# Performance work log

Measured on AMD Instinct MI355X. Metric: run time of the kernel, lower is better.

Reference implementation:

```python
import jax, jax.numpy as jnp
import numpy as np
from jax import lax


def _depthwise_conv1d(x, w, b):
    # x: [B, L, D]; w: [D, 1, KW]; b: [D]
    # Mirrors torch nn.Conv1d(D, D, kernel_size=4, groups=D, padding=3): output length L + 3.
    D = x.shape[-1]
    xt = jnp.transpose(x, (0, 2, 1))  # [B, D, L]
    out = lax.conv_general_dilated(
        xt, w, window_strides=(1,), padding=[(3, 3)],
        feature_group_count=D, dimension_numbers=('NCH', 'OIH', 'NCH'))
    return jnp.transpose(out + b[None, :, None], (0, 2, 1))  # [B, L+3, D]


def _forward(x, a_hat, W_U, W_B, b_B, W_C, b_C, W_d1, b_d1, W_d2, b_d2, D_skip, conv_w, conv_b):
    xc = _depthwise_conv1d(x, conv_w, conv_b)            # [B, Lc, D], Lc = L + 3
    Bsz, Lc, Dm = xc.shape
    S = a_hat.shape[0]
    # selective parameters (torch Linear: y = x @ W.T + b)
    dt_feat = jax.nn.silu(xc @ W_d1.T + b_d1)            # [B, Lc, R]
    delta = jax.nn.softplus(dt_feat @ W_d2.T + b_d2)     # [B, Lc, 1]
    logA = -jnp.exp(a_hat)                               # [S], log(A) <= 0
    A_t = jnp.exp(delta * logA)                          # [B, Lc, S] discretized transition
    u_t = xc @ W_U.T                                     # [B, Lc, S]
    B_t = (xc @ W_B.T + b_B) * u_t                       # [B, Lc, S]
    C_t = xc @ W_C.T + b_C                               # [B, Lc, S]

    # selective scan: h_t = A_t * h_{t-1} + B_t * u_t ; y_t = <C_t, h_t> + D_skip * u_t
    # state h is per-(batch, channel d): [B, D, S]
    def step(h, inp):
        A_l, B_l, C_l, u_l = inp                         # [B,S],[B,S],[B,S],[B,D]
        h = A_l[:, None, :] * h + B_l[:, None, :] * u_l[:, :, None]  # [B, D, S]
        y = jnp.einsum('bds,bs->bd', h, C_l) + D_skip[None, :] * u_l
        return h, y

    h0 = jnp.zeros((Bsz, Dm, S), dtype=xc.dtype)
    _, ys = lax.scan(step, h0, (jnp.swapaxes(A_t, 0, 1), jnp.swapaxes(B_t, 0, 1),
                                jnp.swapaxes(C_t, 0, 1), jnp.swapaxes(xc, 0, 1)))
    return jnp.swapaxes(ys, 0, 1)                        # [B, Lc, D]


def setup_inputs() -> dict:
    key = jax.random.key(0)
    ks = jax.random.split(key, 10)
    B, L, D, S, R, KW = 4, 2048, 1024, 64, 4, 4
    f = jnp.float32
    sc = 0.02
    return {
        'x': jax.random.normal(ks[0], (B, L, D), f),
        'a_hat': jax.random.normal(ks[1], (S,), f),
        'W_U': jax.random.normal(ks[2], (S, D), f) * sc,
        'W_B': jax.random.normal(ks[3], (S, D), f) * sc,
        'b_B': jnp.zeros((S,), f),
        'W_C': jax.random.normal(ks[4], (S, D), f) * sc,
        'b_C': jnp.zeros((S,), f),
        'W_d1': jax.random.normal(ks[5], (R, D), f) * sc,
        'b_d1': jnp.zeros((R,), f),
        'W_d2': jax.random.normal(ks[6], (1, R), f) * sc,
        'b_d2': jnp.zeros((1,), f),
        'D_skip': jax.random.normal(ks[7], (D,), f),
        'conv_w': jax.random.normal(ks[8], (D, 1, KW), f) * 0.25,
        'conv_b': jnp.zeros((D,), f),
    }


def reference(x, a_hat, W_U, W_B, b_B, W_C, b_C, W_d1, b_d1, W_d2, b_d2, D_skip, conv_w, conv_b):
    return _forward(x, a_hat, W_U, W_B, b_B, W_C, b_C, W_d1, b_d1, W_d2, b_d2, D_skip, conv_w, conv_b)
```

## Files before the change

### kernel.cpp

```cpp
#include <hip/hip_runtime.h>
#include <hip/hip_bf16.h>

namespace {
constexpr int kB   = 4;
constexpr int kL   = 2048;
constexpr int kLc  = 2051;
constexpr int kD   = 1024;
constexpr int kS   = 64;
constexpr int kM   = kB * kLc;
constexpr int kNR  = 256;
constexpr int kQ   = 32;
constexpr int kTC  = (kLc + kQ - 1) / kQ;
constexpr int kGA  = 514;
constexpr int kGT  = 16384;
}

typedef __attribute__((ext_vector_type(8))) short bf16x8;
typedef __attribute__((ext_vector_type(4))) float f32x4;
typedef __attribute__((ext_vector_type(8))) unsigned short u16x8;

__device__ __forceinline__ float siluf_(float v) {
  return v / (1.f + expf(-v));
}
__device__ __forceinline__ float softplusf_(float v) {
  return (v > 20.f) ? v : log1pf(expf(v));
}
__device__ __forceinline__ unsigned short f2bf_(float f) {
  unsigned u = __float_as_uint(f);
  unsigned r = u + 0x7FFF + ((u >> 16) & 1);
  return (unsigned short)(r >> 16);
}
__device__ __forceinline__ float bf2f_(unsigned short u) {
  return __uint_as_float(((unsigned)u) << 16);
}

__global__ __launch_bounds__(256) void wcat_kernel(
    const float* __restrict__ W_U, const float* __restrict__ W_B,
    const float* __restrict__ W_C, const float* __restrict__ W_d1,
    unsigned short* __restrict__ wcp, unsigned short* __restrict__ xcp) {
  int g = blockIdx.x;
  int kq = blockIdx.y;
  int tid = threadIdx.x;
  int c8 = tid & 15, r = tid >> 4;
  int n = g * 16 + r;
  int k = kq * 128 + c8 * 8;
  const float* src = nullptr;
  if (n < 64)        src = W_U + (size_t)n * kD;
  else if (n < 128)  src = W_B + (size_t)(n - 64) * kD;
  else if (n < 192)  src = W_C + (size_t)(n - 128) * kD;
  else if (n < 196)  src = W_d1 + (size_t)(n - 192) * kD;
  u16x8 o;
#pragma unroll
  for (int j = 0; j < 8; ++j) o[j] = src ? f2bf_(src[k + j]) : (unsigned short)0;
  size_t dst = (size_t)g * kGT + (size_t)(k >> 5) * 512 + r * 32 + (k & 31);
  *(u16x8*)(wcp + dst) = o;
  if (kq == 0) {
    u16x8 z = {0, 0, 0, 0, 0, 0, 0, 0};
    size_t off = (size_t)512 * kGT + ((size_t)g * 256 + tid) * 8;
    *(u16x8*)(xcp + off) = z;
  }
}

__global__ __launch_bounds__(256) void conv_kernel(
    const float* __restrict__ x, const float* __restrict__ cw,
    const float* __restrict__ cb, unsigned short* __restrict__ xcp,
    unsigned short* __restrict__ xT) {
  __shared__ unsigned short tileT[kQ][136];

  int tid = threadIdx.x;
  int bc = blockIdx.x;
  int d0 = blockIdx.y * 128;
  int b = bc / kTC, c = bc % kTC;
  int t0 = c * kQ;
  int dl = tid & 127, tg = tid >> 7;
  int d = d0 + dl;

  float4 wv = *(const float4*)(cw + (size_t)d * 4);
  float bias = cb[d];
  int tstart = t0 + tg * 16;

  const float* xb = x + (size_t)b * kL * kD + d;
  auto ldx = [&](int t) -> float {
    return (t >= 0 && t < kL) ? xb[(size_t)t * kD] : 0.f;
  };
  float xm3 = ldx(tstart - 3);
  float xm2 = ldx(tstart - 2);
  float xm1 = ldx(tstart - 1);

  unsigned short vals[16];
#pragma unroll
  for (int j = 0; j < 16; ++j) {
    int t = tstart + j;
    float x0 = ldx(t);
    float o = bias + wv.x * xm3 + wv.y * xm2 + wv.z * xm1 + wv.w * x0;
    vals[j] = (t < kLc) ? f2bf_(o) : (unsigned short)0;
    tileT[tg * 16 + j][dl] = vals[j];
    xm3 = xm2; xm2 = xm1; xm1 = x0;
  }
#pragma unroll
  for (int j = 0; j < 16; ++j) {
    int t = tstart + j;
    if (t < kLc) {
      int bt = b * kLc + t;
      size_t po = (size_t)(bt >> 4) * kGT + (size_t)(d >> 5) * 512 +
                  (size_t)(bt & 15) * 32 + (d & 31);
      xcp[po] = vals[j];
    }
  }
  __syncthreads();
  {
    int d_l = tid >> 1, th = tid & 1;
    u16x8 o0, o1;
#pragma unroll
    for (int j = 0; j < 8; ++j) {
      o0[j] = tileT[th * 16 + j][d_l];
      o1[j] = tileT[th * 16 + 8 + j][d_l];
    }
    unsigned short* dst = xT + ((size_t)bc * kD + d0 + d_l) * kQ + th * 16;
    *(u16x8*)dst = o0;
    *(u16x8*)(dst + 8) = o1;
  }
}

__global__ __launch_bounds__(256) void gemm_mfma_kernel(
    const unsigned short* __restrict__ xcp,
    const unsigned short* __restrict__ wcp, float* __restrict__ raw) {
  int tid = threadIdx.x;
  int w = tid >> 6, lane = tid & 63;
  int m0 = blockIdx.x * 32 + (w >> 1) * 16;
  int n0 = blockIdx.y * 128 + (w & 1) * 64;
  int l15 = lane & 15, lk = lane >> 4;

  const unsigned short* ap =
      xcp + (size_t)(blockIdx.x * 2 + (w >> 1)) * kGT + l15 * 32 + lk * 8;
  const unsigned short* bp =
      wcp + (size_t)(blockIdx.y * 8 + (w & 1) * 4) * kGT + l15 * 32 + lk * 8;

  f32x4 acc0 = {0.f, 0.f, 0.f, 0.f}, acc1 = acc0, acc2 = acc0, acc3 = acc0;

  bf16x8 a  = *(const bf16x8*)(ap);
  bf16x8 b0 = *(const bf16x8*)(bp + (size_t)0 * kGT);
  bf16x8 b1 = *(const bf16x8*)(bp + (size_t)1 * kGT);
  bf16x8 b2 = *(const bf16x8*)(bp + (size_t)2 * kGT);
  bf16x8 b3 = *(const bf16x8*)(bp + (size_t)3 * kGT);

#pragma unroll 4
  for (int kt = 1; kt < 32; ++kt) {
    bf16x8 an  = *(const bf16x8*)(ap + kt * 512);
    bf16x8 b0n = *(const bf16x8*)(bp + (size_t)0 * kGT + kt * 512);
    bf16x8 b1n = *(const bf16x8*)(bp + (size_t)1 * kGT + kt * 512);
    bf16x8 b2n = *(const bf16x8*)(bp + (size_t)2 * kGT + kt * 512);
    bf16x8 b3n = *(const bf16x8*)(bp + (size_t)3 * kGT + kt * 512);
    acc0 = __builtin_amdgcn_mfma_f32_16x16x32_bf16(a, b0, acc0, 0, 0, 0);
    acc1 = __builtin_amdgcn_mfma_f32_16x16x32_bf16(a, b1, acc1, 0, 0, 0);
    acc2 = __builtin_amdgcn_mfma_f32_16x16x32_bf16(a, b2, acc2, 0, 0, 0);
    acc3 = __builtin_amdgcn_mfma_f32_16x16x32_bf16(a, b3, acc3, 0, 0, 0);
    a = an; b0 = b0n; b1 = b1n; b2 = b2n; b3 = b3n;
  }
  acc0 = __builtin_amdgcn_mfma_f32_16x16x32_bf16(a, b0, acc0, 0, 0, 0);
  acc1 = __builtin_amdgcn_mfma_f32_16x16x32_bf16(a, b1, acc1, 0, 0, 0);
  acc2 = __builtin_amdgcn_mfma_f32_16x16x32_bf16(a, b2, acc2, 0, 0, 0);
  acc3 = __builtin_amdgcn_mfma_f32_16x16x32_bf16(a, b3, acc3, 0, 0, 0);

  int crow0 = m0 + lk * 4;
  f32x4 accs[4] = {acc0, acc1, acc2, acc3};
#pragma unroll
  for (int nf = 0; nf < 4; ++nf) {
    int col = n0 + nf * 16 + l15;
#pragma unroll
    for (int r = 0; r < 4; ++r) {
      int row = crow0 + r;
      if (row < kM) raw[(size_t)row * kNR + col] = accs[nf][r];
    }
  }
}

__global__ __launch_bounds__(256) void passA_kernel(
    const float* __restrict__ raw,
    const float* __restrict__ b_B, const float* __restrict__ b_C,
    const float* __restrict__ b_d1, const float* __restrict__ W_d2,
    const float* __restrict__ b_d2, const float* __restrict__ a_hat,
    unsigned short* __restrict__ Gm, unsigned short* __restrict__ Ctb,
    unsigned short* __restrict__ Bpre, float* __restrict__ dec) {
  __shared__ __align__(16) float Cfl[32][68];
  __shared__ __align__(16) float BulT[64][36];
  __shared__ float deltal[32];
  __shared__ float Dloc[32];
  __shared__ float logAl[64];

  int tid = threadIdx.x;
  int bc = blockIdx.x;
  int b = bc / kTC, c = bc % kTC;
  int t0 = c * kQ;
  int clen = min(kQ, kLc - t0);

  if (tid < 64) logAl[tid] = -expf(a_hat[tid]);
  if (tid >= 64 && tid < 96) {
    int t = tid - 64;
    float r0 = 0.f, r1 = 0.f, r2 = 0.f, r3 = 0.f;
    if (t < clen) {
      const float* rp = raw + (size_t)(b * kLc + t0 + t) * kNR + 192;
      r0 = rp[0]; r1 = rp[1]; r2 = rp[2]; r3 = rp[3];
    }
    float f0 = siluf_(r0 + b_d1[0]);
    float f1 = siluf_(r1 + b_d1[1]);
    float f2 = siluf_(r2 + b_d1[2]);
    float f3 = siluf_(r3 + b_d1[3]);
    float z = fmaf(f0, W_d2[0],
              fmaf(f1, W_d2[1], fmaf(f2, W_d2[2], fmaf(f3, W_d2[3], b_d2[0]))));
    deltal[t] = softplusf_(z);
  }
  for (int p = 0; p < 8; ++p) {
    int idx = p * 256 + tid;
    int t = idx >> 6, s = idx & 63;
    float u = 0.f, rb = 0.f, rc = 0.f;
    if (t < clen) {
      const float* rp = raw + (size_t)(b * kLc + t0 + t) * kNR;
      u = rp[s]; rb = rp[64 + s]; rc = rp[128 + s];
    }
    BulT[s][t] = (rb + b_B[s]) * u;
    Cfl[t][s] = rc + b_C[s];
  }
  __syncthreads();
  if (tid < 32) {
    float sum = 0.f;
    for (int j = 0; j <= tid; ++j) sum += deltal[j];
    Dloc[tid] = sum;
  }
  __syncthreads();
  float Dend = Dloc[31];

  for (int p = 0; p < 8; ++p) {
    int idx = p * 256 + tid;
    int t = idx >> 6, s = idx & 63;
    Ctb[(size_t)bc * 2048 + t * kS + s] =
        f2bf_(Cfl[t][s] * __expf(Dloc[t] * logAl[s]));
  }
  for (int p = 0; p < 8; ++p) {
    int idx = p * 256 + tid;
    int s = idx >> 5, tau = idx & 31;
    Bpre[(size_t)bc * 2048 + s * kQ + tau] =
        f2bf_(BulT[s][tau] * __expf((Dend - Dloc[tau]) * logAl[s]));
  }
  if (tid < 64) dec[(size_t)bc * kS + tid] = __expf(Dend * logAl[tid]);
  for (int p = 0; p < 4; ++p) {
    int idx = p * 256 + tid;
    int t = idx >> 5, tau = idx & 31;
    float g = 0.f;
    if (tau <= t) {
      float dd = Dloc[t] - Dloc[tau];
      for (int s = 0; s < 64; ++s)
        g = fmaf(Cfl[t][s] * BulT[s][tau], __expf(dd * logAl[s]), g);
    }
    Gm[((size_t)bc * 32 + t) * kQ + tau] = f2bf_(g);
  }
}

__global__ __launch_bounds__(256) void scT_kernel(
    const unsigned short* __restrict__ Bpre, const unsigned short* __restrict__ xT,
    unsigned short* __restrict__ ScT) {
  __shared__ __align__(16) unsigned short Bprel[64][40];
  int tid = threadIdx.x;
  int bc = blockIdx.x;
  int dq = blockIdx.y;
  {
    int s = tid >> 2, c8 = (tid & 3) * 8;
    *(u16x8*)&Bprel[s][c8] = *(const u16x8*)(Bpre + (size_t)bc * 2048 + s * kQ + c8);
  }
  __syncthreads();
  int w = tid >> 6, lane = tid & 63;
  int l15 = lane & 15, lk = lane >> 4;
  bf16x8 bfr[4];
#pragma unroll
  for (int st = 0; st < 4; ++st)
    bfr[st] = *(const bf16x8*)&Bprel[st * 16 + l15][lk * 8];
  const unsigned short* xTb = xT + (size_t)bc * kD * kQ;
  unsigned short* so = ScT + (size_t)bc * kD * kS;
#pragma unroll
  for (int mt = 0; mt < 4; ++mt) {
    int d0t = dq * 256 + (w * 4 + mt) * 16;
    bf16x8 af = *(const bf16x8*)(xTb + (size_t)(d0t + l15) * kQ + lk * 8);
    f32x4 acc[4];
#pragma unroll
    for (int st = 0; st < 4; ++st) {
      f32x4 z = {0.f, 0.f, 0.f, 0.f};
      acc[st] = __builtin_amdgcn_mfma_f32_16x16x32_bf16(af, bfr[st], z, 0, 0, 0);
    }
#pragma unroll
    for (int st = 0; st < 4; ++st)
#pragma unroll
      for (int r = 0; r < 4; ++r)
        so[(size_t)(d0t + lk * 4 + r) * kS + st * 16 + l15] = f2bf_(acc[st][r]);
  }
}

__global__ __launch_bounds__(256) void chscan_kernel(
    const float* __restrict__ dec, unsigned short* __restrict__ Sc) {
  int bk = blockIdx.x >> 7;
  int part = blockIdx.x & 127;
  int p = part * 256 + threadIdx.x;
  int flat = p * 2;
  int s0 = flat & 63;
  const size_t cstride = (size_t)kS * kD;
  size_t base = (size_t)bk * kTC * cstride + flat;
  const float* decb = dec + (size_t)bk * kTC * kS + s0;
  float r0 = 0.f, r1 = 0.f;
  for (int c0 = 0; c0 < kTC; c0 += 16) {
    int n = kTC - c0;
    if (n > 16) n = 16;
    unsigned v[16];
    float2 dd[16];
#pragma unroll
    for (int j = 0; j < 16; ++j) {
      if (j < n) {
        v[j] = *(const unsigned*)(Sc + base + (size_t)(c0 + j) * cstride);
        dd[j] = *(const float2*)(decb + (size_t)(c0 + j) * kS);
      }
    }
#pragma unroll
    for (int j = 0; j < 16; ++j) {
      if (j < n) {
        unsigned ost = (unsigned)f2bf_(r0) | ((unsigned)f2bf_(r1) << 16);
        *(unsigned*)(Sc + base + (size_t)(c0 + j) * cstride) = ost;
        r0 = fmaf(dd[j].x, r0, bf2f_((unsigned short)(v[j] & 0xFFFF)));
        r1 = fmaf(dd[j].y, r1, bf2f_((unsigned short)(v[j] >> 16)));
      }
    }
  }
}

__global__ __launch_bounds__(256) void passB_kernel(
    const unsigned short* __restrict__ Gm, const unsigned short* __restrict__ Ctb,
    const unsigned short* __restrict__ xT, const unsigned short* __restrict__ hT,
    const float* __restrict__ D_skip, float* __restrict__ out) {
  int tid = threadIdx.x;
  int bc = blockIdx.x;
  int quarter = blockIdx.y;
  int b = bc / kTC, c = bc % kTC;
  int t0c = c * kQ;
  int clen = min(kQ, kLc - t0c);
  int w = tid >> 6, lane = tid & 63;
  int l15 = lane & 15, lk = lane >> 4;

  const unsigned short* Gb = Gm + (size_t)bc * 32 * kQ;
  bf16x8 aG0 = *(const bf16x8*)(Gb + (size_t)l15 * kQ + lk * 8);
  bf16x8 aG1 = *(const bf16x8*)(Gb + (size_t)(16 + l15) * kQ + lk * 8);
  const unsigned short* Cb = Ctb + (size_t)bc * 2048;
  bf16x8 aC0l = *(const bf16x8*)(Cb + (size_t)l15 * kS + lk * 8);
  bf16x8 aC0h = *(const bf16x8*)(Cb + (size_t)l15 * kS + 32 + lk * 8);
  bf16x8 aC1l = *(const bf16x8*)(Cb + (size_t)(16 + l15) * kS + lk * 8);
  bf16x8 aC1h = *(const bf16x8*)(Cb + (size_t)(16 + l15) * kS + 32 + lk * 8);

  const unsigned short* xTb = xT + (size_t)bc * kD * kQ;
  const unsigned short* hTb = hT + (size_t)bc * kD * kS;
  size_t rowbase = (size_t)b * kLc + t0c;
  int dbase = quarter * 256 + w * 64;

#pragma unroll
  for (int nt = 0; nt < 4; ++nt) {
    int d = dbase + nt * 16 + l15;
    bf16x8 bX  = *(const bf16x8*)(xTb + (size_t)d * kQ + lk * 8);
    bf16x8 bHl = *(const bf16x8*)(hTb + (size_t)d * kS + lk * 8);
    bf16x8 bHh = *(const bf16x8*)(hTb + (size_t)d * kS + 32 + lk * 8);
    f32x4 z = {0.f, 0.f, 0.f, 0.f};
    f32x4 accA = __builtin_amdgcn_mfma_f32_16x16x32_bf16(aC0l, bHl, z, 0, 0, 0);
    accA = __builtin_amdgcn_mfma_f32_16x16x32_bf16(aC0h, bHh, accA, 0, 0, 0);
    accA = __builtin_amdgcn_mfma_f32_16x16x32_bf16(aG0, bX, accA, 0, 0, 0);
    f32x4 accB = __builtin_amdgcn_mfma_f32_16x16x32_bf16(aC1l, bHl, z, 0, 0, 0);
    accB = __builtin_amdgcn_mfma_f32_16x16x32_bf16(aC1h, bHh, accB, 0, 0, 0);
    accB = __builtin_amdgcn_mfma_f32_16x16x32_bf16(aG1, bX, accB, 0, 0, 0);

    float ds = D_skip[d];
    ushort4 xa = *(const ushort4*)(xTb + (size_t)d * kQ + lk * 4);
    ushort4 xb = *(const ushort4*)(xTb + (size_t)d * kQ + 16 + lk * 4);
    const unsigned short* xap = (const unsigned short*)&xa;
    const unsigned short* xbp = (const unsigned short*)&xb;
#pragma unroll
    for (int r = 0; r < 4; ++r) {
      int t = lk * 4 + r;
      if (t < clen)
        out[(rowbase + t) * kD + d] = fmaf(ds, bf2f_(xap[r]), accA[r]);
      int t2 = 16 + lk * 4 + r;
      if (t2 < clen)
        out[(rowbase + t2) * kD + d] = fmaf(ds, bf2f_(xbp[r]), accB[r]);
    }
  }
}

extern "C" void kernel_launch(void* const* d_in, const int* in_sizes, int n_in,
                              void* d_out, int out_size, void* d_ws, size_t ws_size,
                              hipStream_t stream) {
  const float* x      = (const float*)d_in[0];
  const float* a_hat  = (const float*)d_in[1];
  const float* W_U    = (const float*)d_in[2];
  const float* W_B    = (const float*)d_in[3];
  const float* b_B    = (const float*)d_in[4];
  const float* W_C    = (const float*)d_in[5];
  const float* b_C    = (const float*)d_in[6];
  const float* W_d1   = (const float*)d_in[7];
  const float* b_d1   = (const float*)d_in[8];
  const float* W_d2   = (const float*)d_in[9];
  const float* b_d2   = (const float*)d_in[10];
  const float* D_skip = (const float*)d_in[11];
  const float* conv_w = (const float*)d_in[12];
  const float* conv_b = (const float*)d_in[13];
  float* out = (float*)d_out;

  char* w = (char*)d_ws;
  auto nextp = [&](size_t bytes) {
    char* p = w;
    w += (bytes + 255) & ~(size_t)255;
    return p;
  };
  unsigned short* xcp  = (unsigned short*)nextp((size_t)kGA * kGT * 2);
  unsigned short* wcp  = (unsigned short*)nextp((size_t)16 * kGT * 2);
  unsigned short* xT   = (unsigned short*)nextp((size_t)kB * kTC * kD * kQ * 2);
  float*          raw  = (float*)nextp((size_t)kM * kNR * 4);
  unsigned short* Gm   = (unsigned short*)nextp((size_t)kB * kTC * 32 * kQ * 2);
  unsigned short* Ctb  = (unsigned short*)nextp((size_t)kB * kTC * 2048 * 2);
  unsigned short* Bpre = (unsigned short*)nextp((size_t)kB * kTC * 2048 * 2);
  float*          dec  = (float*)nextp((size_t)kB * kTC * kS * 4);
  unsigned short* ScT  = (unsigned short*)nextp((size_t)kB * kTC * kD * kS * 2);

  dim3 wgrid(16, 8);
  wcat_kernel<<<wgrid, 256, 0, stream>>>(W_U, W_B, W_C, W_d1, wcp, xcp);

  dim3 cgrid(kB * kTC, kD / 128);
  conv_kernel<<<cgrid, 256, 0, stream>>>(x, conv_w, conv_b, xcp, xT);

  dim3 ggrid((kM + 31) / 32, 2);
  gemm_mfma_kernel<<<ggrid, 256, 0, stream>>>(xcp, wcp, raw);

  passA_kernel<<<kB * kTC, 256, 0, stream>>>(
      raw, b_B, b_C, b_d1, W_d2, b_d2, a_hat, Gm, Ctb, Bpre, dec);

  dim3 sgrid(kB * kTC, 4);
  scT_kernel<<<sgrid, 256, 0, stream>>>(Bpre, xT, ScT);

  chscan_kernel<<<kB * 128, 256, 0, stream>>>(dec, ScT);

  dim3 bgrid(kB * kTC, 4);
  passB_kernel<<<bgrid, 256, 0, stream>>>(Gm, Ctb, xT, ScT, D_skip, out);
}
```

Baseline: 111.1 us.

## Fold weight packing into conv kernel and widen GEMM N-tile to full width

Removes the separate weight-conversion launch by giving the conv kernel an extra grid row that packs the weights to bf16 and zeroes the padding rows of the packed activation buffer. The zeroing is narrowed to only the rows conv does not write. The GEMM now covers all 256 output columns per block: each wave holds 8 accumulators instead of 4, so every A fragment is loaded once instead of twice across blocks. This raises register pressure and halves the GEMM grid, which can lower occupancy.

```diff
diff --git a/kernel.cpp b/kernel.cpp
--- a/kernel.cpp
+++ b/kernel.cpp
@@ -34,40 +34,48 @@
   return __uint_as_float(((unsigned)u) << 16);
 }
 
-__global__ __launch_bounds__(256) void wcat_kernel(
-    const float* __restrict__ W_U, const float* __restrict__ W_B,
-    const float* __restrict__ W_C, const float* __restrict__ W_d1,
-    unsigned short* __restrict__ wcp, unsigned short* __restrict__ xcp) {
-  int g = blockIdx.x;
-  int kq = blockIdx.y;
-  int tid = threadIdx.x;
-  int c8 = tid & 15, r = tid >> 4;
-  int n = g * 16 + r;
-  int k = kq * 128 + c8 * 8;
-  const float* src = nullptr;
-  if (n < 64)        src = W_U + (size_t)n * kD;
-  else if (n < 128)  src = W_B + (size_t)(n - 64) * kD;
-  else if (n < 192)  src = W_C + (size_t)(n - 128) * kD;
-  else if (n < 196)  src = W_d1 + (size_t)(n - 192) * kD;
-  u16x8 o;
-#pragma unroll
-  for (int j = 0; j < 8; ++j) o[j] = src ? f2bf_(src[k + j]) : (unsigned short)0;
-  size_t dst = (size_t)g * kGT + (size_t)(k >> 5) * 512 + r * 32 + (k & 31);
-  *(u16x8*)(wcp + dst) = o;
-  if (kq == 0) {
-    u16x8 z = {0, 0, 0, 0, 0, 0, 0, 0};
-    size_t off = (size_t)512 * kGT + ((size_t)g * 256 + tid) * 8;
-    *(u16x8*)(xcp + off) = z;
-  }
-}
-
 __global__ __launch_bounds__(256) void conv_kernel(
     const float* __restrict__ x, const float* __restrict__ cw,
     const float* __restrict__ cb, unsigned short* __restrict__ xcp,
-    unsigned short* __restrict__ xT) {
+    unsigned short* __restrict__ xT,
+    const float* __restrict__ W_U, const float* __restrict__ W_B,
+    const float* __restrict__ W_C, const float* __restrict__ W_d1,
+    unsigned short* __restrict__ wcp) {
   __shared__ unsigned short tileT[kQ][136];
 
   int tid = threadIdx.x;
+  if (blockIdx.y == 8) {
+    int bx = blockIdx.x;
+    if (bx < 128) {
+      int g = bx >> 3, kq = bx & 7;
+      int c8 = tid & 15, r = tid >> 4;
+      int n = g * 16 + r;
+      int k = kq * 128 + c8 * 8;
+      const float* src = nullptr;
+      if (n < 64)        src = W_U + (size_t)n * kD;
+      else if (n < 128)  src = W_B + (size_t)(n - 64) * kD;
+      else if (n < 192)  src = W_C + (size_t)(n - 128) * kD;
+      else if (n < 196)  src = W_d1 + (size_t)(n - 192) * kD;
+      u16x8 o;
+#pragma unroll
+      for (int j = 0; j < 8; ++j)
+        o[j] = src ? f2bf_(src[k + j]) : (unsigned short)0;
+      size_t dst = (size_t)g * kGT + (size_t)(k >> 5) * 512 + r * 32 + (k & 31);
+      *(u16x8*)(wcp + dst) = o;
+    } else if (bx < 136) {
+      u16x8 z = {0, 0, 0, 0, 0, 0, 0, 0};
+      size_t off = (size_t)513 * kGT + (size_t)(bx - 128) * 2048 + (size_t)tid * 8;
+      *(u16x8*)(xcp + off) = z;
+    } else if (bx < 138) {
+      int i = (bx - 136) * 256 + tid;
+      int kt = i >> 4, rr = (i >> 2) & 3, k8 = i & 3;
+      u16x8 z = {0, 0, 0, 0, 0, 0, 0, 0};
+      size_t off = (size_t)512 * kGT + (size_t)kt * 512 + (12 + rr) * 32 + k8 * 8;
+      *(u16x8*)(xcp + off) = z;
+    }
+    return;
+  }
+
   int bc = blockIdx.x;
   int d0 = blockIdx.y * 128;
   int b = bc / kTC, c = bc % kTC;
@@ -128,49 +136,49 @@
   int tid = threadIdx.x;
   int w = tid >> 6, lane = tid & 63;
   int m0 = blockIdx.x * 32 + (w >> 1) * 16;
-  int n0 = blockIdx.y * 128 + (w & 1) * 64;
+  int n0 = (w & 1) * 128;
   int l15 = lane & 15, lk = lane >> 4;
 
   const unsigned short* ap =
       xcp + (size_t)(blockIdx.x * 2 + (w >> 1)) * kGT + l15 * 32 + lk * 8;
   const unsigned short* bp =
-      wcp + (size_t)(blockIdx.y * 8 + (w & 1) * 4) * kGT + l15 * 32 + lk * 8;
-
-  f32x4 acc0 = {0.f, 0.f, 0.f, 0.f}, acc1 = acc0, acc2 = acc0, acc3 = acc0;
-
-  bf16x8 a  = *(const bf16x8*)(ap);
-  bf16x8 b0 = *(const bf16x8*)(bp + (size_t)0 * kGT);
-  bf16x8 b1 = *(const bf16x8*)(bp + (size_t)1 * kGT);
-  bf16x8 b2 = *(const bf16x8*)(bp + (size_t)2 * kGT);
-  bf16x8 b3 = *(const bf16x8*)(bp + (size_t)3 * kGT);
-
-#pragma unroll 4
+      wcp + (size_t)((w & 1) * 8) * kGT + l15 * 32 + lk * 8;
+
+  f32x4 acc[8];
+#pragma unroll
+  for (int nf = 0; nf < 8; ++nf) acc[nf] = f32x4{0.f, 0.f, 0.f, 0.f};
+
+  bf16x8 a = *(const bf16x8*)(ap);
+  bf16x8 bfr[8];
+#pragma unroll
+  for (int nf = 0; nf < 8; ++nf)
+    bfr[nf] = *(const bf16x8*)(bp + (size_t)nf * kGT);
+
   for (int kt = 1; kt < 32; ++kt) {
-    bf16x8 an  = *(const bf16x8*)(ap + kt * 512);
-    bf16x8 b0n = *(const bf16x8*)(bp + (size_t)0 * kGT + kt * 512);
-    bf16x8 b1n = *(const bf16x8*)(bp + (size_t)1 * kGT + kt * 512);
-    bf16x8 b2n = *(const bf16x8*)(bp + (size_t)2 * kGT + kt * 512);
-    bf16x8 b3n = *(const bf16x8*)(bp + (size_t)3 * kGT + kt * 512);
-    acc0 = __builtin_amdgcn_mfma_f32_16x16x32_bf16(a, b0, acc0, 0, 0, 0);
-    acc1 = __builtin_amdgcn_mfma_f32_16x16x32_bf16(a, b1, acc1, 0, 0, 0);
-    acc2 = __builtin_amdgcn_mfma_f32_16x16x32_bf16(a, b2, acc2, 0, 0, 0);
-    acc3 = __builtin_amdgcn_mfma_f32_16x16x32_bf16(a, b3, acc3, 0, 0, 0);
-    a = an; b0 = b0n; b1 = b1n; b2 = b2n; b3 = b3n;
-  }
-  acc0 = __builtin_amdgcn_mfma_f32_16x16x32_bf16(a, b0, acc0, 0, 0, 0);
-  acc1 = __builtin_amdgcn_mfma_f32_16x16x32_bf16(a, b1, acc1, 0, 0, 0);
-  acc2 = __builtin_amdgcn_mfma_f32_16x16x32_bf16(a, b2, acc2, 0, 0, 0);
-  acc3 = __builtin_amdgcn_mfma_f32_16x16x32_bf16(a, b3, acc3, 0, 0, 0);
+    bf16x8 an = *(const bf16x8*)(ap + kt * 512);
+    bf16x8 bn[8];
+#pragma unroll
+    for (int nf = 0; nf < 8; ++nf)
+      bn[nf] = *(const bf16x8*)(bp + (size_t)nf * kGT + kt * 512);
+#pragma unroll
+    for (int nf = 0; nf < 8; ++nf)
+      acc[nf] = __builtin_amdgcn_mfma_f32_16x16x32_bf16(a, bfr[nf], acc[nf], 0, 0, 0);
+    a = an;
+#pragma unroll
+    for (int nf = 0; nf < 8; ++nf) bfr[nf] = bn[nf];
+  }
+#pragma unroll
+  for (int nf = 0; nf < 8; ++nf)
+    acc[nf] = __builtin_amdgcn_mfma_f32_16x16x32_bf16(a, bfr[nf], acc[nf], 0, 0, 0);
 
   int crow0 = m0 + lk * 4;
-  f32x4 accs[4] = {acc0, acc1, acc2, acc3};
-#pragma unroll
-  for (int nf = 0; nf < 4; ++nf) {
+#pragma unroll
+  for (int nf = 0; nf < 8; ++nf) {
     int col = n0 + nf * 16 + l15;
 #pragma unroll
     for (int r = 0; r < 4; ++r) {
       int row = crow0 + r;
-      if (row < kM) raw[(size_t)row * kNR + col] = accs[nf][r];
+      if (row < kM) raw[(size_t)row * kNR + col] = acc[nf][r];
     }
   }
 }
@@ -422,14 +430,11 @@
   float*          dec  = (float*)nextp((size_t)kB * kTC * kS * 4);
   unsigned short* ScT  = (unsigned short*)nextp((size_t)kB * kTC * kD * kS * 2);
 
-  dim3 wgrid(16, 8);
-  wcat_kernel<<<wgrid, 256, 0, stream>>>(W_U, W_B, W_C, W_d1, wcp, xcp);
-
-  dim3 cgrid(kB * kTC, kD / 128);
-  conv_kernel<<<cgrid, 256, 0, stream>>>(x, conv_w, conv_b, xcp, xT);
-
-  dim3 ggrid((kM + 31) / 32, 2);
-  gemm_mfma_kernel<<<ggrid, 256, 0, stream>>>(xcp, wcp, raw);
+  dim3 cgrid(kB * kTC, 9);
+  conv_kernel<<<cgrid, 256, 0, stream>>>(x, conv_w, conv_b, xcp, xT,
+                                         W_U, W_B, W_C, W_d1, wcp);
+
+  gemm_mfma_kernel<<<(kM + 31) / 32, 256, 0, stream>>>(xcp, wcp, raw);
 
   passA_kernel<<<kB * kTC, 256, 0, stream>>>(
       raw, b_B, b_C, b_d1, W_d2, b_d2, a_hat, Gm, Ctb, Bpre, dec);
```

Result: no change. 111.1 us (+0.0%).
